# Optimization experiments

Measured on AMD Instinct MI355X. Metric: run time of the kernel, lower is better.

The kernel has to match this reference:

```python
import jax, jax.numpy as jnp
import numpy as np

S, B, C = 7, 2, 20
LAMBDA_COORD, LAMBDA_NOOBJ = 5.0, 0.5
N_BATCH = 8192
OBJ_PROB = 0.05


def setup_inputs() -> dict:
    key = jax.random.key(0)
    k_pred, k_tgt, k_obj = jax.random.split(key, 3)
    pred = jax.random.normal(k_pred, (N_BATCH, S * S * (5 * B + C)), dtype=jnp.float32)
    # target cells: [conf, x, y, w, h, 20 class scores]; conf must be exactly 0/1
    tgt = jax.random.uniform(k_tgt, (N_BATCH * S * S, 5 + C), dtype=jnp.float32)
    obj = jax.random.bernoulli(k_obj, OBJ_PROB, (N_BATCH * S * S,)).astype(jnp.float32)
    tgt = tgt.at[:, 0].set(obj)
    target = tgt.reshape(N_BATCH, S * S * (5 + C))
    return {"pred": pred, "target": target}


def _to_xyxy(xywh, gy, gx):
    # xywh: [..., 4]; gy/gx broadcastable to leading dims
    cx = (gx + xywh[..., 0]) / S
    cy = (gy + xywh[..., 1]) / S
    w = xywh[..., 2]
    h = xywh[..., 3]
    return jnp.stack([cx - w / 2, cy - h / 2, cx + w / 2, cy + h / 2], axis=-1)


def _yolo_loss(pred, target):
    N = pred.shape[0]
    p = pred.reshape(-1, 5 * B + C)          # [M, 30], M = N*S*S
    t = target.reshape(-1, 5 + C)            # [M, 25]
    M = p.shape[0]
    objf = (t[:, 0] == 1.0).astype(p.dtype)
    noobjf = (t[:, 0] == 0.0).astype(p.dtype)

    boxes = p[:, : 5 * B].reshape(M, B, 5)   # [M, B, 5] (conf, x, y, w, h)
    tbox = t[:, :5]                           # [M, 5]

    grid = jnp.tile(jnp.arange(S * S), M // (S * S))
    gy = (grid // 7).astype(p.dtype)
    gx = (grid % 7).astype(p.dtype)

    # IoU matching (pred wh taken as abs, matching .square().sqrt())
    pb = jnp.abs(boxes[..., 1:5])                             # [M, B, 4]
    pxyxy = _to_xyxy(pb, gy[:, None], gx[:, None])            # [M, B, 4]
    txyxy = _to_xyxy(tbox[:, 1:5], gy, gx)                    # [M, 4]

    lt = jnp.maximum(pxyxy[..., :2], txyxy[:, None, :2])
    rb = jnp.minimum(pxyxy[..., 2:], txyxy[:, None, 2:])
    wh = jnp.clip(rb - lt, 0.0)
    inter = wh[..., 0] * wh[..., 1]                           # [M, B]
    area_p = (pxyxy[..., 2] - pxyxy[..., 0]) * (pxyxy[..., 3] - pxyxy[..., 1])
    area_t = (txyxy[..., 2] - txyxy[..., 0]) * (txyxy[..., 3] - txyxy[..., 1])
    iou = inter / (area_p + area_t[:, None] - inter)          # [M, B]

    best = jnp.argmax(iou, axis=1)                            # first max on ties, like torch
    max_iou = jnp.max(iou, axis=1)                            # [M]
    resp = jnp.take_along_axis(boxes, best[:, None, None], axis=1)[:, 0]  # [M, 5]

    # localization (raw pred xy; sqrt(abs(wh)))
    xy_loss = jnp.sum(objf[:, None] * (resp[:, 1:3] - tbox[:, 1:3]) ** 2)
    pw = jnp.sqrt(jnp.abs(resp[:, 3:5]))
    tw = jnp.sqrt(jnp.abs(tbox[:, 3:5]))
    wh_loss = jnp.sum(objf[:, None] * (pw - tw) ** 2)
    localization = LAMBDA_COORD * (xy_loss + wh_loss)

    # confidence: responsible box conf vs IoU (IoU NOT detached, as in source)
    obj_conf = jnp.sum(objf * (resp[:, 0] - max_iou) ** 2)
    noobj_conf = LAMBDA_NOOBJ * jnp.sum(noobjf[:, None] * boxes[:, :, 0] ** 2)

    cls_loss = jnp.sum(objf[:, None] * (p[:, -C:] - t[:, -C:]) ** 2)

    return (localization + obj_conf + noobj_conf + cls_loss) / N


def reference(pred, target):
    return _yolo_loss(pred, target)
```

## Files before the change

### kernel.cpp

```cpp
#include <hip/hip_runtime.h>


#define NBATCH  8192
#define PSTRIDE 30
#define TSTRIDE 25
#define TPB     64
#define NCHUNKS 6272

__global__ __launch_bounds__(TPB) void yolo_partial_kernel(
    const float* __restrict__ pred,
    const float* __restrict__ tgt,
    float* __restrict__ partials)
{
    __shared__ float sp[TPB * PSTRIDE];
    __shared__ float st[TPB * TSTRIDE];

    const int lane = threadIdx.x;
    const size_t c0 = (size_t)blockIdx.x * TPB;

    const float4* gp = (const float4*)(pred + c0 * PSTRIDE);
    float4* lp = (float4*)sp;
    #pragma unroll
    for (int k = 0; k < 7; ++k)
        lp[lane + k * TPB] = gp[lane + k * TPB];
    if (lane < 32)
        lp[lane + 7 * TPB] = gp[lane + 7 * TPB];

    const float4* gt = (const float4*)(tgt + c0 * TSTRIDE);
    float4* lt = (float4*)st;
    #pragma unroll
    for (int k = 0; k < 6; ++k)
        lt[lane + k * TPB] = gt[lane + k * TPB];
    if (lane < 16)
        lt[lane + 6 * TPB] = gt[lane + 6 * TPB];


    const float* p = sp + lane * PSTRIDE;
    const float* t = st + lane * TSTRIDE;

    int cell = (int)((c0 + lane) % 49);
    float gy = (float)(cell / 7);
    float gx = (float)(cell % 7);
    const float invS = 1.0f / 7.0f;

    float t0 = t[0], tx = t[1], ty = t[2], tw = t[3], th = t[4];
    float objf   = (t0 == 1.0f) ? 1.0f : 0.0f;
    float noobjf = (t0 == 0.0f) ? 1.0f : 0.0f;

    float tcx = (gx + tx) * invS, tcy = (gy + ty) * invS;
    float tx1 = tcx - tw * 0.5f, ty1 = tcy - th * 0.5f;
    float tx2 = tcx + tw * 0.5f, ty2 = tcy + th * 0.5f;
    float area_t = (tx2 - tx1) * (ty2 - ty1);

    float conf[2], bx[2], by[2], bw[2], bh[2], iou[2];
    #pragma unroll
    for (int b = 0; b < 2; ++b) {
        conf[b] = p[b * 5 + 0];
        bx[b]   = p[b * 5 + 1];
        by[b]   = p[b * 5 + 2];
        bw[b]   = p[b * 5 + 3];
        bh[b]   = p[b * 5 + 4];
        float ax = fabsf(bx[b]), ay = fabsf(by[b]);
        float aw = fabsf(bw[b]), ah = fabsf(bh[b]);
        float cx = (gx + ax) * invS, cy = (gy + ay) * invS;
        float x1 = cx - aw * 0.5f, y1 = cy - ah * 0.5f;
        float x2 = cx + aw * 0.5f, y2 = cy + ah * 0.5f;
        float ltx = fmaxf(x1, tx1), lty = fmaxf(y1, ty1);
        float rbx = fminf(x2, tx2), rby = fminf(y2, ty2);
        float wx = fmaxf(rbx - ltx, 0.0f);
        float wy = fmaxf(rby - lty, 0.0f);
        float inter = wx * wy;
        float area_p = (x2 - x1) * (y2 - y1);
        iou[b] = inter / (area_p + area_t - inter);
    }

    int best = (iou[1] > iou[0]) ? 1 : 0;
    float miou = fmaxf(iou[0], iou[1]);

    float rc = conf[best];
    float rx = bx[best], ry = by[best], rw = bw[best], rh = bh[best];

    float dx = rx - tx, dy = ry - ty;
    float sw = sqrtf(fabsf(rw)) - sqrtf(fabsf(tw));
    float sh = sqrtf(fabsf(rh)) - sqrtf(fabsf(th));
    float loc = dx * dx + dy * dy + sw * sw + sh * sh;

    float oc = rc - miou;
    oc = oc * oc;

    float no = conf[0] * conf[0] + conf[1] * conf[1];

    float cls = 0.0f;
    #pragma unroll
    for (int k = 0; k < 20; ++k) {
        float d = p[10 + k] - t[5 + k];
        cls += d * d;
    }

    float part = objf * (5.0f * loc + oc + cls) + 0.5f * noobjf * no;

    #pragma unroll
    for (int off = 32; off > 0; off >>= 1)
        part += __shfl_down(part, off, 64);
    if (lane == 0)
        partials[blockIdx.x] = part;
}

__global__ __launch_bounds__(256) void yolo_final_kernel(
    const float* __restrict__ partials,
    float* __restrict__ out, float invN)
{
    const int tid = threadIdx.x;
    float s = 0.0f;
    for (int i = tid; i < NCHUNKS; i += 256)
        s += partials[i];
    #pragma unroll
    for (int off = 32; off > 0; off >>= 1)
        s += __shfl_down(s, off, 64);
    __shared__ float ws[4];
    int lane = tid & 63, wid = tid >> 6;
    if (lane == 0) ws[wid] = s;
    __syncthreads();
    if (tid == 0)
        out[0] = (ws[0] + ws[1] + ws[2] + ws[3]) * invN;
}

extern "C" void kernel_launch(void* const* d_in, const int* in_sizes, int n_in,
                              void* d_out, int out_size, void* d_ws, size_t ws_size,
                              hipStream_t stream) {
    const float* pred = (const float*)d_in[0];
    const float* tgt  = (const float*)d_in[1];
    float* out = (float*)d_out;
    float* partials = (float*)d_ws;

    yolo_partial_kernel<<<NCHUNKS, TPB, 0, stream>>>(pred, tgt, partials);
    yolo_final_kernel<<<1, 256, 0, stream>>>(partials, out, 1.0f / (float)NBATCH);
}
```

Measured before the change: 27.22 us.

## Double-buffer direct global-to-LDS loads, two cell chunks per block

Each 64-thread block now handles two 64-cell chunks. Both chunks are staged with global_load_lds async copies into two shared buffers, so the first chunk can be computed while the second is still loading, controlled by vmcnt waits. This halves the number of blocks and partials, and the final reduction loop is unrolled. It depends on the vmcnt(15) count matching the number of load instructions issued, and it doubles LDS per block, which may lower occupancy.

```diff
diff --git a/kernel.cpp b/kernel.cpp
--- a/kernel.cpp
+++ b/kernel.cpp
@@ -5,40 +5,22 @@
 #define PSTRIDE 30
 #define TSTRIDE 25
 #define TPB     64
-#define NCHUNKS 6272
+#define CPB     128
+#define NBLOCKS 3136
+#define PBYTES  (64 * PSTRIDE * 4)
+#define TBYTES  (64 * TSTRIDE * 4)
 
-__global__ __launch_bounds__(TPB) void yolo_partial_kernel(
-    const float* __restrict__ pred,
-    const float* __restrict__ tgt,
-    float* __restrict__ partials)
+__device__ __forceinline__ void gll16(const void* g, void* l) {
+    __builtin_amdgcn_global_load_lds(
+        (const __attribute__((address_space(1))) void*)g,
+        (__attribute__((address_space(3))) void*)l,
+        16, 0, 0);
+}
+
+__device__ __forceinline__ float cell_loss(const float* __restrict__ p,
+                                           const float* __restrict__ t,
+                                           int cell)
 {
-    __shared__ float sp[TPB * PSTRIDE];
-    __shared__ float st[TPB * TSTRIDE];
-
-    const int lane = threadIdx.x;
-    const size_t c0 = (size_t)blockIdx.x * TPB;
-
-    const float4* gp = (const float4*)(pred + c0 * PSTRIDE);
-    float4* lp = (float4*)sp;
-    #pragma unroll
-    for (int k = 0; k < 7; ++k)
-        lp[lane + k * TPB] = gp[lane + k * TPB];
-    if (lane < 32)
-        lp[lane + 7 * TPB] = gp[lane + 7 * TPB];
-
-    const float4* gt = (const float4*)(tgt + c0 * TSTRIDE);
-    float4* lt = (float4*)st;
-    #pragma unroll
-    for (int k = 0; k < 6; ++k)
-        lt[lane + k * TPB] = gt[lane + k * TPB];
-    if (lane < 16)
-        lt[lane + 6 * TPB] = gt[lane + 6 * TPB];
-
-
-    const float* p = sp + lane * PSTRIDE;
-    const float* t = st + lane * TSTRIDE;
-
-    int cell = (int)((c0 + lane) % 49);
     float gy = (float)(cell / 7);
     float gx = (float)(cell % 7);
     const float invS = 1.0f / 7.0f;
@@ -97,7 +79,64 @@
         cls += d * d;
     }
 
-    float part = objf * (5.0f * loc + oc + cls) + 0.5f * noobjf * no;
+    return objf * (5.0f * loc + oc + cls) + 0.5f * noobjf * no;
+}
+
+__global__ __launch_bounds__(TPB) void yolo_partial_kernel(
+    const float* __restrict__ pred,
+    const float* __restrict__ tgt,
+    float* __restrict__ partials)
+{
+    __shared__ __align__(16) float sp[2][64 * PSTRIDE];
+    __shared__ __align__(16) float st[2][64 * TSTRIDE];
+
+    const int lane = threadIdx.x;
+    const size_t cell0 = (size_t)blockIdx.x * CPB;
+
+    const char* gp = (const char*)(pred + cell0 * PSTRIDE);
+    const char* gt = (const char*)(tgt  + cell0 * TSTRIDE);
+
+    {
+        char* lp = (char*)sp[0];
+        #pragma unroll
+        for (int s = 0; s < 7; ++s)
+            gll16(gp + s * 1024 + lane * 16, lp + s * 1024 + lane * 16);
+        if (lane < 32)
+            gll16(gp + 7 * 1024 + lane * 16, lp + 7 * 1024 + lane * 16);
+        char* lt = (char*)st[0];
+        #pragma unroll
+        for (int s = 0; s < 6; ++s)
+            gll16(gt + s * 1024 + lane * 16, lt + s * 1024 + lane * 16);
+        if (lane < 16)
+            gll16(gt + 6 * 1024 + lane * 16, lt + 6 * 1024 + lane * 16);
+    }
+    asm volatile("" ::: "memory");
+    {
+        const char* gpb = gp + PBYTES;
+        const char* gtb = gt + TBYTES;
+        char* lp = (char*)sp[1];
+        #pragma unroll
+        for (int s = 0; s < 7; ++s)
+            gll16(gpb + s * 1024 + lane * 16, lp + s * 1024 + lane * 16);
+        if (lane < 32)
+            gll16(gpb + 7 * 1024 + lane * 16, lp + 7 * 1024 + lane * 16);
+        char* lt = (char*)st[1];
+        #pragma unroll
+        for (int s = 0; s < 6; ++s)
+            gll16(gtb + s * 1024 + lane * 16, lt + s * 1024 + lane * 16);
+        if (lane < 16)
+            gll16(gtb + 6 * 1024 + lane * 16, lt + 6 * 1024 + lane * 16);
+    }
+
+    asm volatile("s_waitcnt vmcnt(15)" ::: "memory");
+    __builtin_amdgcn_sched_barrier(0);
+    float part = cell_loss(&sp[0][lane * PSTRIDE], &st[0][lane * TSTRIDE],
+                           (int)((cell0 + lane) % 49));
+
+    asm volatile("s_waitcnt vmcnt(0)" ::: "memory");
+    __builtin_amdgcn_sched_barrier(0);
+    part += cell_loss(&sp[1][lane * PSTRIDE], &st[1][lane * TSTRIDE],
+                      (int)((cell0 + 64 + lane) % 49));
 
     #pragma unroll
     for (int off = 32; off > 0; off >>= 1)
@@ -112,8 +151,11 @@
 {
     const int tid = threadIdx.x;
     float s = 0.0f;
-    for (int i = tid; i < NCHUNKS; i += 256)
-        s += partials[i];
+    #pragma unroll
+    for (int k = 0; k < 13; ++k) {
+        int i = tid + k * 256;
+        if (i < NBLOCKS) s += partials[i];
+    }
     #pragma unroll
     for (int off = 32; off > 0; off >>= 1)
         s += __shfl_down(s, off, 64);
@@ -133,6 +175,6 @@
     float* out = (float*)d_out;
     float* partials = (float*)d_ws;
 
-    yolo_partial_kernel<<<NCHUNKS, TPB, 0, stream>>>(pred, tgt, partials);
+    yolo_partial_kernel<<<NBLOCKS, TPB, 0, stream>>>(pred, tgt, partials);
     yolo_final_kernel<<<1, 256, 0, stream>>>(partials, out, 1.0f / (float)NBATCH);
 }
```

Measured after the change: 23.86 us. 1.14x faster.
